# Kernel tuning notes

Measured on AMD Instinct MI355X. Metric: run time of the kernel, lower is better.

Reference implementation:

```python
import jax, jax.numpy as jnp
import numpy as np

N_NODES = 50000
N_EDGES = 800000
D = 64
D_OUT = 64


def setup_inputs() -> dict:
    key = jax.random.key(0)
    ks = jax.random.split(key, 7)
    h_src = jax.random.normal(ks[0], (N_NODES, D), dtype=jnp.float32)
    h_dst = jax.random.normal(ks[1], (N_NODES, D), dtype=jnp.float32)
    e = jax.random.normal(ks[2], (N_EDGES, D), dtype=jnp.float32)
    src = jax.random.randint(ks[3], (N_EDGES,), 0, N_NODES, dtype=jnp.int32)
    dst = jax.random.randint(ks[4], (N_EDGES,), 0, N_NODES, dtype=jnp.int32)
    W = jax.random.normal(ks[5], (D_OUT, 2 * D), dtype=jnp.float32) * 0.05  # nn.Linear weight [out, in]
    b = jax.random.normal(ks[6], (D_OUT,), dtype=jnp.float32) * 0.05
    return {"h_src": h_src, "h_dst": h_dst, "e": e, "src": src, "dst": dst, "W": W, "b": b}


def reference(h_src, h_dst, e, src, dst, W, b):
    # u_dot_e: per-edge dot product between gathered src features and edge features
    h_u = h_src[src]                                   # [E, D] gather
    score = jnp.sum(h_u * e, axis=-1)                  # [E]
    exp_s = jnp.exp(score)                             # raw exp, as in original (no max-subtract)
    # segment-sum exp over dst nodes, then edge-wise normalize (edge softmax)
    denom = jax.ops.segment_sum(exp_s, dst, num_segments=N_NODES)  # [N]
    pi = exp_s / denom[dst]                            # [E]
    # weighted neighbor aggregation: sum_e pi * h_src[src] into dst
    msg = h_u * pi[:, None]                            # [E, D]
    h_sum = jax.ops.segment_sum(msg, dst, num_segments=N_NODES)    # [N, D]
    # concat self features with aggregated neighbors, then linear
    h_total = jnp.concatenate([h_dst, h_sum], axis=1)  # [N, 2D]
    return h_total @ W.T + b                           # [N, D_OUT]
```

## Files before the change

kernel.cpp:

```cpp
#include <hip/hip_runtime.h>

#define N_NODES 50000
#define N_EDGES 800000
#define D 64
#define CAP 64

typedef float vf4 __attribute__((ext_vector_type(4)));

__global__ __launch_bounds__(256) void k1_score_bucket(
    const vf4* __restrict__ h_src4, const vf4* __restrict__ e4,
    const int* __restrict__ src, const int* __restrict__ dst,
    int* __restrict__ count, int2* __restrict__ slots) {
    int t = threadIdx.x;
    int i = blockIdx.x * 16 + (t >> 4);
    int l16 = t & 15;
    int s = src[i];
    vf4 u  = h_src4[(size_t)s * 16 + l16];
    vf4 ev = e4[(size_t)i * 16 + l16];
    float p = u[0]*ev[0] + u[1]*ev[1] + u[2]*ev[2] + u[3]*ev[3];
    p += __shfl_xor(p, 1, 16);
    p += __shfl_xor(p, 2, 16);
    p += __shfl_xor(p, 4, 16);
    p += __shfl_xor(p, 8, 16);
    if (l16 == 0) {
        int d = dst[i];
        float w = __expf(p);
        int pos = atomicAdd(&count[d], 1);
        if (pos < CAP)
            slots[(size_t)d * CAP + pos] = make_int2(s, __float_as_int(w));
    }
}

__global__ __launch_bounds__(256, 6) void k2_agg(
    const vf4* __restrict__ h_src4,
    const int* __restrict__ count, const int2* __restrict__ slots,
    vf4* __restrict__ h_sum4) {
    int t = threadIdx.x;
    int node = blockIdx.x * 16 + (t >> 4);
    int l16 = t & 15;
    int cnt = count[node];
    cnt = cnt < CAP ? cnt : CAP;
    const int2* row = slots + (size_t)node * CAP;
    vf4 acc = {0.f, 0.f, 0.f, 0.f};
    float dsum = 0.f;
    int2 se = make_int2(0, 0);
    if (l16 < cnt) se = row[l16];
    for (int base = 0; base < cnt; base += 16) {
        int2 cur = se;
        int nxt = base + 16;
        se = make_int2(0, 0);
        if (nxt + l16 < cnt) se = row[nxt + l16];
        #pragma unroll
        for (int j = 0; j < 16; ++j) {
            int sj = __shfl(cur.x, j, 16);
            float wj = __int_as_float(__shfl(cur.y, j, 16));
            vf4 u = h_src4[(size_t)sj * 16 + l16];
            acc += wj * u;
            dsum += wj;
        }
    }
    float inv = (cnt > 0) ? 1.f / dsum : 0.f;
    acc *= inv;
    h_sum4[(size_t)node * 16 + l16] = acc;
}

__global__ __launch_bounds__(256) void k3_linear(
    const vf4* __restrict__ h_dst4, const vf4* __restrict__ h_sum4,
    const float* __restrict__ W, const float* __restrict__ b,
    float* __restrict__ out) {
    __shared__ float Wl[128 * 65];
    __shared__ __align__(16) float ht[16][132];
    int t = threadIdx.x;
    for (int i = t; i < 128 * 64; i += 256) {
        int o = i >> 7, k = i & 127;
        Wl[k * 65 + o] = W[i];
    }
    int node0 = blockIdx.x * 16;
    {
        int n = t >> 4;
        int l16 = t & 15;
        int node = node0 + n;
        vf4 hd = h_dst4[(size_t)node * 16 + l16];
        vf4 hs = h_sum4[(size_t)node * 16 + l16];
        *(vf4*)&ht[n][l16 * 4] = hd;
        *(vf4*)&ht[n][64 + l16 * 4] = hs;
    }
    __syncthreads();

    int o = t & 63;
    int g = t >> 6;
    float bias = b[o];
    float a0 = bias, a1 = bias, a2 = bias, a3 = bias;
    const float* h0 = &ht[g * 4 + 0][0];
    const float* h1 = &ht[g * 4 + 1][0];
    const float* h2 = &ht[g * 4 + 2][0];
    const float* h3 = &ht[g * 4 + 3][0];
    #pragma unroll
    for (int k = 0; k < 128; k += 4) {
        float w0 = Wl[(k + 0) * 65 + o];
        float w1 = Wl[(k + 1) * 65 + o];
        float w2 = Wl[(k + 2) * 65 + o];
        float w3 = Wl[(k + 3) * 65 + o];
        vf4 p0 = *(const vf4*)&h0[k];
        vf4 p1 = *(const vf4*)&h1[k];
        vf4 p2 = *(const vf4*)&h2[k];
        vf4 p3 = *(const vf4*)&h3[k];
        a0 += p0[0]*w0 + p0[1]*w1 + p0[2]*w2 + p0[3]*w3;
        a1 += p1[0]*w0 + p1[1]*w1 + p1[2]*w2 + p1[3]*w3;
        a2 += p2[0]*w0 + p2[1]*w1 + p2[2]*w2 + p2[3]*w3;
        a3 += p3[0]*w0 + p3[1]*w1 + p3[2]*w2 + p3[3]*w3;
    }
    out[(size_t)(node0 + g * 4 + 0) * 64 + o] = a0;
    out[(size_t)(node0 + g * 4 + 1) * 64 + o] = a1;
    out[(size_t)(node0 + g * 4 + 2) * 64 + o] = a2;
    out[(size_t)(node0 + g * 4 + 3) * 64 + o] = a3;
}

extern "C" void kernel_launch(void* const* d_in, const int* in_sizes, int n_in,
                              void* d_out, int out_size, void* d_ws, size_t ws_size,
                              hipStream_t stream) {
    const float* h_src = (const float*)d_in[0];
    const float* h_dst = (const float*)d_in[1];
    const float* e     = (const float*)d_in[2];
    const int*   src   = (const int*)d_in[3];
    const int*   dst   = (const int*)d_in[4];
    const float* W     = (const float*)d_in[5];
    const float* b     = (const float*)d_in[6];
    float* out = (float*)d_out;

    auto align256 = [](size_t x) { return (x + 255) & ~(size_t)255; };
    char* ws = (char*)d_ws;
    int*  count = (int*)ws;
    int2* slots = (int2*)(ws + align256((size_t)N_NODES * 4));
    float* h_sum = (float*)(ws + align256((size_t)N_NODES * 4)
                               + align256((size_t)N_NODES * CAP * 8));

    hipMemsetAsync(count, 0, (size_t)N_NODES * 4, stream);

    k1_score_bucket<<<N_EDGES / 16, 256, 0, stream>>>(
        (const vf4*)h_src, (const vf4*)e, src, dst, count, slots);
    k2_agg<<<N_NODES / 16, 256, 0, stream>>>(
        (const vf4*)h_src, count, slots, (vf4*)h_sum);
    k3_linear<<<(N_NODES + 15) / 16, 256, 0, stream>>>(
        (const vf4*)h_dst, (const vf4*)h_sum, W, b, out);
}
```

Baseline: 380.8 us.

## Fuse aggregation and linear kernels, batch gathers, use nontemporal loads and stores

Merges the per-node aggregation kernel with the linear-layer kernel, so the aggregated features go straight into shared memory and the h_sum round trip through global memory and one launch are removed. The gather loop now issues all 16 neighbor loads before accumulating, to raise memory-level parallelism. It also adds nontemporal loads for edge features and nontemporal stores for the output, and hoists the dst load. In exchange, every fused block now loads the full 128x64 weight matrix into shared memory, and the larger shared-memory footprint plus the register-held gather batch may lower occupancy of the latency-bound gather.

```diff
diff --git a/kernel.cpp b/kernel.cpp
--- a/kernel.cpp
+++ b/kernel.cpp
@@ -15,15 +15,15 @@
     int i = blockIdx.x * 16 + (t >> 4);
     int l16 = t & 15;
     int s = src[i];
+    int d = dst[i];
     vf4 u  = h_src4[(size_t)s * 16 + l16];
-    vf4 ev = e4[(size_t)i * 16 + l16];
+    vf4 ev = __builtin_nontemporal_load(&e4[(size_t)i * 16 + l16]);
     float p = u[0]*ev[0] + u[1]*ev[1] + u[2]*ev[2] + u[3]*ev[3];
     p += __shfl_xor(p, 1, 16);
     p += __shfl_xor(p, 2, 16);
     p += __shfl_xor(p, 4, 16);
     p += __shfl_xor(p, 8, 16);
     if (l16 == 0) {
-        int d = dst[i];
         float w = __expf(p);
         int pos = atomicAdd(&count[d], 1);
         if (pos < CAP)
@@ -31,13 +31,24 @@
     }
 }
 
-__global__ __launch_bounds__(256, 6) void k2_agg(
-    const vf4* __restrict__ h_src4,
+__global__ __launch_bounds__(256) void k23_agg_linear(
+    const vf4* __restrict__ h_src4, const vf4* __restrict__ h_dst4,
     const int* __restrict__ count, const int2* __restrict__ slots,
-    vf4* __restrict__ h_sum4) {
+    const float* __restrict__ W, const float* __restrict__ b,
+    float* __restrict__ out) {
+    __shared__ float Wl[128 * 65];
+    __shared__ __align__(16) float ht[16][132];
     int t = threadIdx.x;
-    int node = blockIdx.x * 16 + (t >> 4);
+    for (int i = t; i < 128 * 64; i += 256) {
+        int o = i >> 7, k = i & 127;
+        Wl[k * 65 + o] = W[i];
+    }
+    int node0 = blockIdx.x * 16;
+    int n = t >> 4;
     int l16 = t & 15;
+    int node = node0 + n;
+    *(vf4*)&ht[n][l16 * 4] = h_dst4[(size_t)node * 16 + l16];
+
     int cnt = count[node];
     cnt = cnt < CAP ? cnt : CAP;
     const int2* row = slots + (size_t)node * CAP;
@@ -50,41 +61,22 @@
         int nxt = base + 16;
         se = make_int2(0, 0);
         if (nxt + l16 < cnt) se = row[nxt + l16];
+        vf4 us[16];
         #pragma unroll
         for (int j = 0; j < 16; ++j) {
             int sj = __shfl(cur.x, j, 16);
+            us[j] = h_src4[(size_t)sj * 16 + l16];
+        }
+        #pragma unroll
+        for (int j = 0; j < 16; ++j) {
             float wj = __int_as_float(__shfl(cur.y, j, 16));
-            vf4 u = h_src4[(size_t)sj * 16 + l16];
-            acc += wj * u;
+            acc += wj * us[j];
             dsum += wj;
         }
     }
     float inv = (cnt > 0) ? 1.f / dsum : 0.f;
     acc *= inv;
-    h_sum4[(size_t)node * 16 + l16] = acc;
-}
-
-__global__ __launch_bounds__(256) void k3_linear(
-    const vf4* __restrict__ h_dst4, const vf4* __restrict__ h_sum4,
-    const float* __restrict__ W, const float* __restrict__ b,
-    float* __restrict__ out) {
-    __shared__ float Wl[128 * 65];
-    __shared__ __align__(16) float ht[16][132];
-    int t = threadIdx.x;
-    for (int i = t; i < 128 * 64; i += 256) {
-        int o = i >> 7, k = i & 127;
-        Wl[k * 65 + o] = W[i];
-    }
-    int node0 = blockIdx.x * 16;
-    {
-        int n = t >> 4;
-        int l16 = t & 15;
-        int node = node0 + n;
-        vf4 hd = h_dst4[(size_t)node * 16 + l16];
-        vf4 hs = h_sum4[(size_t)node * 16 + l16];
-        *(vf4*)&ht[n][l16 * 4] = hd;
-        *(vf4*)&ht[n][64 + l16 * 4] = hs;
-    }
+    *(vf4*)&ht[n][64 + l16 * 4] = acc;
     __syncthreads();
 
     int o = t & 63;
@@ -110,10 +102,10 @@
         a2 += p2[0]*w0 + p2[1]*w1 + p2[2]*w2 + p2[3]*w3;
         a3 += p3[0]*w0 + p3[1]*w1 + p3[2]*w2 + p3[3]*w3;
     }
-    out[(size_t)(node0 + g * 4 + 0) * 64 + o] = a0;
-    out[(size_t)(node0 + g * 4 + 1) * 64 + o] = a1;
-    out[(size_t)(node0 + g * 4 + 2) * 64 + o] = a2;
-    out[(size_t)(node0 + g * 4 + 3) * 64 + o] = a3;
+    __builtin_nontemporal_store(a0, &out[(size_t)(node0 + g * 4 + 0) * 64 + o]);
+    __builtin_nontemporal_store(a1, &out[(size_t)(node0 + g * 4 + 1) * 64 + o]);
+    __builtin_nontemporal_store(a2, &out[(size_t)(node0 + g * 4 + 2) * 64 + o]);
+    __builtin_nontemporal_store(a3, &out[(size_t)(node0 + g * 4 + 3) * 64 + o]);
 }
 
 extern "C" void kernel_launch(void* const* d_in, const int* in_sizes, int n_in,
@@ -132,15 +124,11 @@
     char* ws = (char*)d_ws;
     int*  count = (int*)ws;
     int2* slots = (int2*)(ws + align256((size_t)N_NODES * 4));
-    float* h_sum = (float*)(ws + align256((size_t)N_NODES * 4)
-                               + align256((size_t)N_NODES * CAP * 8));
 
     hipMemsetAsync(count, 0, (size_t)N_NODES * 4, stream);
 
     k1_score_bucket<<<N_EDGES / 16, 256, 0, stream>>>(
         (const vf4*)h_src, (const vf4*)e, src, dst, count, slots);
-    k2_agg<<<N_NODES / 16, 256, 0, stream>>>(
-        (const vf4*)h_src, count, slots, (vf4*)h_sum);
-    k3_linear<<<(N_NODES + 15) / 16, 256, 0, stream>>>(
-        (const vf4*)h_dst, (const vf4*)h_sum, W, b, out);
+    k23_agg_linear<<<N_NODES / 16, 256, 0, stream>>>(
+        (const vf4*)h_src, (const vf4*)h_dst, count, slots, W, b, out);
 }
```

After: 381.7 us. About the same (+0.3%).
